# Kernel optimization log

Measured on AMD Instinct MI355X. Metric: run time of the kernel, lower is better.

## Reference

```python
import jax, jax.numpy as jnp
import numpy as np

B, T, F = 16, 2048, 512


def setup_inputs() -> dict:
    key = jax.random.key(0)
    k1, k2, k3 = jax.random.split(key, 3)
    x = jax.random.normal(k1, (B, T, F), dtype=jnp.float32)
    w_aggr = jax.random.normal(k2, (F, 1), dtype=jnp.float32) * 0.02
    b_aggr = jnp.zeros((1,), dtype=jnp.float32)
    # lengths in [T//2, T] to avoid degenerate lengths[0]==0 (torch would div by 0 too)
    seq_len = jax.random.randint(k3, (B,), T // 2, T + 1).astype(jnp.int32)
    return {"x": x, "w_aggr": w_aggr, "b_aggr": b_aggr, "seq_len": seq_len}


def reference(x, w_aggr, b_aggr, seq_len):
    """Valley-detection dynamic segment-mean pooling.

    Faithful to the torch code, but the O(T^2) triangular-mask bmm is
    expressed as the mathematically identical prefix-sum difference:
    bmm(utri[end]-utri[start], v) == cumsum(v)[end] - cumsum(v)[start].
    Output time dim is padded to T (>= dynamic max_counts); padded segment
    rows have start==end==0 -> numerator 0 / clamp -> exactly 0, matching
    the torch zero-padded `valleys` rows.
    """
    Bx, Tx, Fx = x.shape
    wt = jax.nn.sigmoid(x @ w_aggr + b_aggr)[..., 0]          # [B,T] gate weights
    before = jnp.pad(wt[:, :-1], ((0, 0), (1, 0)))            # pad 0 (sigmoid>0 => pos 0 never valley)
    after = jnp.pad(wt[:, 1:], ((0, 0), (0, 1)))              # pad 0 => pos T-1 never valley
    valley = (wt < before) & (wt < after)                     # [B,T] strict local minima
    starts_mask = valley.at[:, 0].set(True)                   # mask[:,0]=True
    ends_mask = valley.at[:, 0].set(False).at[:, -1].set(True)  # mask[:,0]=False; mask[:,-1]=True

    t = jnp.arange(Tx, dtype=jnp.int32)
    bi = jnp.arange(Bx)[:, None]

    def pack(m, vals):
        # left-pack values at True positions into fixed [B,T] (zeros beyond count)
        rank = jnp.cumsum(m, axis=1) - 1
        slot = jnp.where(m, rank, Tx)                         # dump non-selected into slot T
        out = jnp.zeros((Bx, Tx + 1), jnp.int32).at[bi, slot].set(vals)
        return out[:, :Tx], jnp.sum(m, axis=1)

    starts, counts = pack(starts_mask, jnp.broadcast_to(t, (Bx, Tx)))
    end_vals = jnp.broadcast_to(jnp.minimum(t + 2, Tx), (Bx, Tx))  # valley_index_end clipped to length
    ends, _ = pack(ends_mask, end_vals)

    alpha_h = wt[..., None] * x                               # [B,T,F]
    # exclusive->inclusive prefix sums with leading zero row
    cs_ah = jnp.concatenate([jnp.zeros((Bx, 1, Fx), x.dtype), jnp.cumsum(alpha_h, axis=1)], axis=1)
    cs_w = jnp.concatenate([jnp.zeros((Bx, 1), x.dtype), jnp.cumsum(wt, axis=1)], axis=1)

    num = cs_ah[bi, ends] - cs_ah[bi, starts]                 # [B,T,F] segment sums of w*x
    den = jnp.clip(cs_w[bi, ends] - cs_w[bi, starts], 1e-6, None)[..., None]
    pooled = num / den                                        # weighted segment mean

    max_counts = jnp.max(counts)
    lengths = jnp.minimum(seq_len, Tx)
    new_lengths = (lengths.astype(jnp.float32) / lengths[0].astype(jnp.float32)
                   * max_counts.astype(jnp.float32)).astype(jnp.int32)
    new_mask = t[None, :] < new_lengths[:, None]              # [B,T]
    return pooled, new_mask
```

## Files before the change

kernel.cpp:

```cpp
#include <hip/hip_runtime.h>
#include <math.h>

#define BB 16
#define TT 2048
#define FF 512

__global__ __launch_bounds__(256) void wt_kernel(const float* __restrict__ x,
                                                 const float* __restrict__ w,
                                                 const float* __restrict__ bias,
                                                 float* __restrict__ wt) {
    int gid  = blockIdx.x * 256 + threadIdx.x;
    int row  = gid >> 6;
    int lane = gid & 63;
    const float* xr = x + (size_t)row * FF + lane * 8;
    const float* wr = w + lane * 8;
    float4 a0 = *(const float4*)xr;
    float4 a1 = *(const float4*)(xr + 4);
    float4 w0 = *(const float4*)wr;
    float4 w1 = *(const float4*)(wr + 4);
    float s = a0.x * w0.x + a0.y * w0.y + a0.z * w0.z + a0.w * w0.w
            + a1.x * w1.x + a1.y * w1.y + a1.z * w1.z + a1.w * w1.w;
#pragma unroll
    for (int off = 32; off > 0; off >>= 1) s += __shfl_xor(s, off, 64);
    if (lane == 0) {
        float z = s + bias[0];
        wt[row] = 1.0f / (1.0f + expf(-z));
    }
}

__global__ __launch_bounds__(256) void seg_kernel(const float* __restrict__ wt,
                                                  int* __restrict__ starts,
                                                  int* __restrict__ ends,
                                                  int* __restrict__ counts) {
    int b   = blockIdx.x;
    int tid = threadIdx.x;
    __shared__ float sw[TT];
    __shared__ int   scan[256];
    const float* wrow = wt + b * TT;
    for (int i = tid; i < TT; i += 256) sw[i] = wrow[i];
    __syncthreads();

    int base = tid * 8;
    int flags = 0, cnt = 0;
#pragma unroll
    for (int k = 0; k < 8; ++k) {
        int t = base + k;
        bool v = (t > 0) && (t < TT - 1) && (sw[t] < sw[t - 1]) && (sw[t] < sw[t + 1]);
        if (v) { flags |= (1 << k); ++cnt; }
    }
    scan[tid] = cnt;
    __syncthreads();
    for (int off = 1; off < 256; off <<= 1) {
        int add = (tid >= off) ? scan[tid - off] : 0;
        __syncthreads();
        scan[tid] += add;
        __syncthreads();
    }
    int total = scan[255];
    int r = scan[tid] - cnt;
    int* sb = starts + b * TT;
    int* eb = ends + b * TT;
#pragma unroll
    for (int k = 0; k < 8; ++k) {
        if (flags & (1 << k)) {
            int t = base + k;
            sb[r + 1] = t;
            int e = t + 2; if (e > TT) e = TT;
            eb[r] = e;
            ++r;
        }
    }
    if (tid == 0) {
        sb[0] = 0;
        eb[total] = TT;
        counts[b] = total + 1;
    }
}

__global__ __launch_bounds__(256) void pool_kernel(const float* __restrict__ x,
                                                   const float* __restrict__ wt,
                                                   const int* __restrict__ starts,
                                                   const int* __restrict__ ends,
                                                   const int* __restrict__ counts,
                                                   float* __restrict__ out) {
    int gid  = blockIdx.x * 256 + threadIdx.x;
    int row  = gid >> 6;
    int lane = gid & 63;
    int b = row >> 11;
    int j = row & (TT - 1);
    float4 acc0 = make_float4(0.f, 0.f, 0.f, 0.f);
    float4 acc1 = make_float4(0.f, 0.f, 0.f, 0.f);
    if (j < counts[b]) {
        int s = starts[row], e = ends[row];
        const float* xb   = x + (size_t)b * TT * FF + lane * 8;
        const float* wrow = wt + b * TT;
        float den = 0.f;
        for (int t = s; t < e; ++t) {
            float wv = wrow[t];
            const float4* p = (const float4*)(xb + (size_t)t * FF);
            float4 v0 = p[0], v1 = p[1];
            acc0.x += wv * v0.x; acc0.y += wv * v0.y;
            acc0.z += wv * v0.z; acc0.w += wv * v0.w;
            acc1.x += wv * v1.x; acc1.y += wv * v1.y;
            acc1.z += wv * v1.z; acc1.w += wv * v1.w;
            den += wv;
        }
        float inv = 1.0f / fmaxf(den, 1e-6f);
        acc0.x *= inv; acc0.y *= inv; acc0.z *= inv; acc0.w *= inv;
        acc1.x *= inv; acc1.y *= inv; acc1.z *= inv; acc1.w *= inv;
    }
    float* orow = out + (size_t)row * FF + lane * 8;
    *(float4*)orow = acc0;
    *(float4*)(orow + 4) = acc1;
}

__global__ __launch_bounds__(256) void mask_kernel(const int* __restrict__ counts,
                                                   const int* __restrict__ seq_len,
                                                   float* __restrict__ mask_out) {
    int idx = blockIdx.x * 256 + threadIdx.x;
    int b = idx >> 11;
    int t = idx & (TT - 1);
    int maxc = 0;
#pragma unroll
    for (int i = 0; i < BB; ++i) maxc = max(maxc, counts[i]);
    int len_b = min(seq_len[b], TT);
    int len0  = min(seq_len[0], TT);
    int nl = (int)((float)len_b / (float)len0 * (float)maxc);
    mask_out[idx] = (t < nl) ? 1.0f : 0.0f;
}

extern "C" void kernel_launch(void* const* d_in, const int* in_sizes, int n_in,
                              void* d_out, int out_size, void* d_ws, size_t ws_size,
                              hipStream_t stream) {
    const float* x       = (const float*)d_in[0];
    const float* w_aggr  = (const float*)d_in[1];
    const float* b_aggr  = (const float*)d_in[2];
    const int*   seq_len = (const int*)d_in[3];

    float* pooled = (float*)d_out;
    float* mask   = (float*)d_out + (size_t)BB * TT * FF;

    float* wt    = (float*)d_ws;
    int* starts  = (int*)((char*)d_ws + (size_t)BB * TT * 4);
    int* ends    = starts + BB * TT;
    int* counts  = ends + BB * TT;

    const int rows = BB * TT;
    wt_kernel<<<rows / 4, 256, 0, stream>>>(x, w_aggr, b_aggr, wt);
    seg_kernel<<<BB, 256, 0, stream>>>(wt, starts, ends, counts);
    pool_kernel<<<rows / 4, 256, 0, stream>>>(x, wt, starts, ends, counts, pooled);
    mask_kernel<<<rows / 256, 256, 0, stream>>>(counts, seq_len, mask);
}
```

Before: 131.2 us.

## Rewrite segment scan as single-wavefront shuffle scan and fuse mask into pool kernel

The valley-detection kernel now uses one 64-lane wavefront per batch row. Each lane holds 32 gate values in registers, gets its neighbours through shuffles and runs a shuffle-based prefix scan, so the shared-memory scan and its __syncthreads barriers are gone. The mask computation is folded into the pool kernel as extra trailing blocks, which saves one kernel launch. The cost is a serial per-lane loop over the set bits and a larger per-thread register footprint in the seg kernel.

```diff
diff --git a/kernel.cpp b/kernel.cpp
--- a/kernel.cpp
+++ b/kernel.cpp
@@ -4,6 +4,8 @@
 #define BB 16
 #define TT 2048
 #define FF 512
+#define POOL_BLOCKS ((BB * TT) / 4)
+#define MASK_BLOCKS ((BB * TT) / 256)
 
 __global__ __launch_bounds__(256) void wt_kernel(const float* __restrict__ x,
                                                  const float* __restrict__ w,
@@ -28,62 +30,81 @@
     }
 }
 
-__global__ __launch_bounds__(256) void seg_kernel(const float* __restrict__ wt,
-                                                  int* __restrict__ starts,
-                                                  int* __restrict__ ends,
-                                                  int* __restrict__ counts) {
-    int b   = blockIdx.x;
-    int tid = threadIdx.x;
-    __shared__ float sw[TT];
-    __shared__ int   scan[256];
+__global__ __launch_bounds__(64) void seg_kernel(const float* __restrict__ wt,
+                                                 int* __restrict__ starts,
+                                                 int* __restrict__ ends,
+                                                 int* __restrict__ counts) {
+    int b    = blockIdx.x;
+    int lane = threadIdx.x;
     const float* wrow = wt + b * TT;
-    for (int i = tid; i < TT; i += 256) sw[i] = wrow[i];
-    __syncthreads();
-
-    int base = tid * 8;
-    int flags = 0, cnt = 0;
+    float v[32];
+    const float4* p = (const float4*)(wrow + lane * 32);
 #pragma unroll
     for (int k = 0; k < 8; ++k) {
-        int t = base + k;
-        bool v = (t > 0) && (t < TT - 1) && (sw[t] < sw[t - 1]) && (sw[t] < sw[t + 1]);
-        if (v) { flags |= (1 << k); ++cnt; }
+        float4 f = p[k];
+        v[4*k] = f.x; v[4*k+1] = f.y; v[4*k+2] = f.z; v[4*k+3] = f.w;
     }
-    scan[tid] = cnt;
-    __syncthreads();
-    for (int off = 1; off < 256; off <<= 1) {
-        int add = (tid >= off) ? scan[tid - off] : 0;
-        __syncthreads();
-        scan[tid] += add;
-        __syncthreads();
+    float left  = __shfl_up(v[31], 1, 64);
+    float right = __shfl_down(v[0], 1, 64);
+    unsigned int flags = 0;
+#pragma unroll
+    for (int k = 0; k < 32; ++k) {
+        int t = lane * 32 + k;
+        float prev = (k == 0)  ? left  : v[k - 1];
+        float next = (k == 31) ? right : v[k + 1];
+        bool val = (t > 0) && (t < TT - 1) && (v[k] < prev) && (v[k] < next);
+        if (val) flags |= (1u << k);
     }
-    int total = scan[255];
-    int r = scan[tid] - cnt;
+    int cnt = __popc(flags);
+    int inc = cnt;
+#pragma unroll
+    for (int off = 1; off < 64; off <<= 1) {
+        int y = __shfl_up(inc, off, 64);
+        if (lane >= off) inc += y;
+    }
+    int total = __shfl(inc, 63, 64);
+    int r = inc - cnt;
     int* sb = starts + b * TT;
     int* eb = ends + b * TT;
-#pragma unroll
-    for (int k = 0; k < 8; ++k) {
-        if (flags & (1 << k)) {
-            int t = base + k;
-            sb[r + 1] = t;
-            int e = t + 2; if (e > TT) e = TT;
-            eb[r] = e;
-            ++r;
-        }
+    unsigned int f = flags;
+    while (f) {
+        int k = __ffs(f) - 1;
+        f &= f - 1;
+        int t = lane * 32 + k;
+        sb[r + 1] = t;
+        eb[r] = t + 2;
+        ++r;
     }
-    if (tid == 0) {
+    if (lane == 0) {
         sb[0] = 0;
         eb[total] = TT;
         counts[b] = total + 1;
     }
 }
 
-__global__ __launch_bounds__(256) void pool_kernel(const float* __restrict__ x,
-                                                   const float* __restrict__ wt,
-                                                   const int* __restrict__ starts,
-                                                   const int* __restrict__ ends,
-                                                   const int* __restrict__ counts,
-                                                   float* __restrict__ out) {
-    int gid  = blockIdx.x * 256 + threadIdx.x;
+__global__ __launch_bounds__(256) void pool_mask_kernel(const float* __restrict__ x,
+                                                        const float* __restrict__ wt,
+                                                        const int* __restrict__ starts,
+                                                        const int* __restrict__ ends,
+                                                        const int* __restrict__ counts,
+                                                        const int* __restrict__ seq_len,
+                                                        float* __restrict__ out,
+                                                        float* __restrict__ mask_out) {
+    int blk = blockIdx.x;
+    if (blk >= POOL_BLOCKS) {
+        int idx = (blk - POOL_BLOCKS) * 256 + threadIdx.x;
+        int b = idx >> 11;
+        int t = idx & (TT - 1);
+        int maxc = 0;
+#pragma unroll
+        for (int i = 0; i < BB; ++i) maxc = max(maxc, counts[i]);
+        int len_b = min(seq_len[b], TT);
+        int len0  = min(seq_len[0], TT);
+        int nl = (int)((float)len_b / (float)len0 * (float)maxc);
+        mask_out[idx] = (t < nl) ? 1.0f : 0.0f;
+        return;
+    }
+    int gid  = blk * 256 + threadIdx.x;
     int row  = gid >> 6;
     int lane = gid & 63;
     int b = row >> 11;
@@ -114,21 +135,6 @@
     *(float4*)(orow + 4) = acc1;
 }
 
-__global__ __launch_bounds__(256) void mask_kernel(const int* __restrict__ counts,
-                                                   const int* __restrict__ seq_len,
-                                                   float* __restrict__ mask_out) {
-    int idx = blockIdx.x * 256 + threadIdx.x;
-    int b = idx >> 11;
-    int t = idx & (TT - 1);
-    int maxc = 0;
-#pragma unroll
-    for (int i = 0; i < BB; ++i) maxc = max(maxc, counts[i]);
-    int len_b = min(seq_len[b], TT);
-    int len0  = min(seq_len[0], TT);
-    int nl = (int)((float)len_b / (float)len0 * (float)maxc);
-    mask_out[idx] = (t < nl) ? 1.0f : 0.0f;
-}
-
 extern "C" void kernel_launch(void* const* d_in, const int* in_sizes, int n_in,
                               void* d_out, int out_size, void* d_ws, size_t ws_size,
                               hipStream_t stream) {
@@ -147,7 +153,7 @@
 
     const int rows = BB * TT;
     wt_kernel<<<rows / 4, 256, 0, stream>>>(x, w_aggr, b_aggr, wt);
-    seg_kernel<<<BB, 256, 0, stream>>>(wt, starts, ends, counts);
-    pool_kernel<<<rows / 4, 256, 0, stream>>>(x, wt, starts, ends, counts, pooled);
-    mask_kernel<<<rows / 256, 256, 0, stream>>>(counts, seq_len, mask);
+    seg_kernel<<<BB, 64, 0, stream>>>(wt, starts, ends, counts);
+    pool_mask_kernel<<<POOL_BLOCKS + MASK_BLOCKS, 256, 0, stream>>>(
+        x, wt, starts, ends, counts, seq_len, pooled, mask);
 }
```

Measured after the change: 128.7 us. Within noise of the previous version (-1.9%).

## Fuse segmentation, pooling and mask into one kernel with per-block valley scan

Applied to the files above, without the earlier changes.

Replaces the separate segmentation, pooling and mask kernels with one fused kernel. Each pooling block recomputes its batch row's valley flags and prefix scan in shared memory using wave shuffles, then finds its segment bounds by binary search. This removes the starts/ends workspace round trip, two launches and the serialized 16-block scan kernel. Block 0 computes the counts and writes the mask. Rows at index 1024 and above get nontemporal zero stores, because valleys cannot be adjacent and so there are at most 1024 segments. The cost is redundant scan work repeated in every block.

```diff
diff --git a/kernel.cpp b/kernel.cpp
--- a/kernel.cpp
+++ b/kernel.cpp
@@ -4,6 +4,9 @@
 #define BB 16
 #define TT 2048
 #define FF 512
+#define POOL_BLOCKS 8192
+
+typedef float v4f __attribute__((ext_vector_type(4)));
 
 __global__ __launch_bounds__(256) void wt_kernel(const float* __restrict__ x,
                                                  const float* __restrict__ w,
@@ -28,105 +31,133 @@
     }
 }
 
-__global__ __launch_bounds__(256) void seg_kernel(const float* __restrict__ wt,
-                                                  int* __restrict__ starts,
-                                                  int* __restrict__ ends,
-                                                  int* __restrict__ counts) {
-    int b   = blockIdx.x;
+__global__ __launch_bounds__(256) void pool_mask_kernel(const float* __restrict__ x,
+                                                        const float* __restrict__ wt,
+                                                        const int* __restrict__ seq_len,
+                                                        float* __restrict__ out,
+                                                        float* __restrict__ mask_out) {
+    int blk = blockIdx.x;
     int tid = threadIdx.x;
+
+    if (blk == 0) {
+        __shared__ int cnt16[BB];
+        __shared__ int nl16[BB];
+        if (tid < BB) cnt16[tid] = 0;
+        __syncthreads();
+        int br = tid >> 4;
+        int t0 = (tid & 15) * 128;
+        const float* wr = wt + br * TT;
+        int c = 0;
+        for (int k = 0; k < 128; ++k) {
+            int t = t0 + k;
+            if (t > 0 && t < TT - 1) {
+                float cv = wr[t];
+                if (cv < wr[t - 1] && cv < wr[t + 1]) ++c;
+            }
+        }
+        atomicAdd(&cnt16[br], c);
+        __syncthreads();
+        int maxc = 0;
+#pragma unroll
+        for (int i = 0; i < BB; ++i) maxc = max(maxc, cnt16[i] + 1);
+        if (tid < BB) {
+            int len_b = min(seq_len[tid], TT);
+            int len0  = min(seq_len[0], TT);
+            nl16[tid] = (int)((float)len_b / (float)len0 * (float)maxc);
+        }
+        __syncthreads();
+        for (int i = tid; i < BB * TT; i += 256) {
+            int bb = i >> 11, t = i & (TT - 1);
+            mask_out[i] = (t < nl16[bb]) ? 1.0f : 0.0f;
+        }
+        return;
+    }
+
+    int pb   = blk - 1;
+    int b    = pb >> 9;
+    int j0   = (pb & 511) * 4;
+    int lane = tid & 63;
+    int wv   = tid >> 6;
+    int row  = b * TT + j0 + wv;
+    float* orow = out + (size_t)row * FF + lane * 8;
+    v4f zero = (v4f)(0.f);
+
+    if (j0 >= 1024) {
+        __builtin_nontemporal_store(zero, (v4f*)orow);
+        __builtin_nontemporal_store(zero, (v4f*)(orow + 4));
+        return;
+    }
+
     __shared__ float sw[TT];
-    __shared__ int   scan[256];
+    __shared__ int   sflag[256];
+    __shared__ int   sexcl[256];
+    __shared__ int   swsum[4];
     const float* wrow = wt + b * TT;
-    for (int i = tid; i < TT; i += 256) sw[i] = wrow[i];
+    ((v4f*)sw)[tid]       = ((const v4f*)wrow)[tid];
+    ((v4f*)sw)[tid + 256] = ((const v4f*)wrow)[tid + 256];
     __syncthreads();
 
+    unsigned int flags = 0;
     int base = tid * 8;
-    int flags = 0, cnt = 0;
 #pragma unroll
     for (int k = 0; k < 8; ++k) {
         int t = base + k;
-        bool v = (t > 0) && (t < TT - 1) && (sw[t] < sw[t - 1]) && (sw[t] < sw[t + 1]);
-        if (v) { flags |= (1 << k); ++cnt; }
+        float c = sw[t];
+        bool v = (t > 0) && (t < TT - 1) && (c < sw[t - 1]) && (c < sw[t + 1]);
+        if (v) flags |= (1u << k);
     }
-    scan[tid] = cnt;
+    int cnt = __popc(flags);
+    sflag[tid] = (int)flags;
+    int inc = cnt;
+#pragma unroll
+    for (int off = 1; off < 64; off <<= 1) {
+        int y = __shfl_up(inc, off, 64);
+        if (lane >= off) inc += y;
+    }
+    if (lane == 63) swsum[wv] = inc;
+    sexcl[tid] = inc - cnt;
     __syncthreads();
-    for (int off = 1; off < 256; off <<= 1) {
-        int add = (tid >= off) ? scan[tid - off] : 0;
-        __syncthreads();
-        scan[tid] += add;
-        __syncthreads();
-    }
-    int total = scan[255];
-    int r = scan[tid] - cnt;
-    int* sb = starts + b * TT;
-    int* eb = ends + b * TT;
-#pragma unroll
-    for (int k = 0; k < 8; ++k) {
-        if (flags & (1 << k)) {
-            int t = base + k;
-            sb[r + 1] = t;
-            int e = t + 2; if (e > TT) e = TT;
-            eb[r] = e;
-            ++r;
-        }
-    }
-    if (tid == 0) {
-        sb[0] = 0;
-        eb[total] = TT;
-        counts[b] = total + 1;
-    }
-}
+    int woff = 0;
+    for (int i = 0; i < 4; ++i) if (i < wv) woff += swsum[i];
+    int myexcl = sexcl[tid] + woff;
+    __syncthreads();
+    sexcl[tid] = myexcl;
+    __syncthreads();
+    int Vtot = sexcl[255] + __popc((unsigned)sflag[255]);
 
-__global__ __launch_bounds__(256) void pool_kernel(const float* __restrict__ x,
-                                                   const float* __restrict__ wt,
-                                                   const int* __restrict__ starts,
-                                                   const int* __restrict__ ends,
-                                                   const int* __restrict__ counts,
-                                                   float* __restrict__ out) {
-    int gid  = blockIdx.x * 256 + threadIdx.x;
-    int row  = gid >> 6;
-    int lane = gid & 63;
-    int b = row >> 11;
-    int j = row & (TT - 1);
-    float4 acc0 = make_float4(0.f, 0.f, 0.f, 0.f);
-    float4 acc1 = make_float4(0.f, 0.f, 0.f, 0.f);
-    if (j < counts[b]) {
-        int s = starts[row], e = ends[row];
-        const float* xb   = x + (size_t)b * TT * FF + lane * 8;
-        const float* wrow = wt + b * TT;
+    int j = j0 + wv;
+    v4f acc0 = (v4f)(0.f);
+    v4f acc1 = (v4f)(0.f);
+    bool active = (j <= Vtot);
+    if (active) {
+        auto nth_valley = [&](int rho) -> int {
+            int lo = 0, hi = 255;
+            while (lo < hi) {
+                int mid = (lo + hi + 1) >> 1;
+                if (sexcl[mid] <= rho) lo = mid; else hi = mid - 1;
+            }
+            unsigned int f = (unsigned)sflag[lo];
+            int r = rho - sexcl[lo];
+            while (r--) f &= f - 1;
+            return lo * 8 + (__ffs(f) - 1);
+        };
+        int s = (j == 0) ? 0 : nth_valley(j - 1);
+        int e = (j < Vtot) ? nth_valley(j) + 2 : TT;
+        const float* xb = x + (size_t)b * TT * FF + lane * 8;
         float den = 0.f;
         for (int t = s; t < e; ++t) {
-            float wv = wrow[t];
-            const float4* p = (const float4*)(xb + (size_t)t * FF);
-            float4 v0 = p[0], v1 = p[1];
-            acc0.x += wv * v0.x; acc0.y += wv * v0.y;
-            acc0.z += wv * v0.z; acc0.w += wv * v0.w;
-            acc1.x += wv * v1.x; acc1.y += wv * v1.y;
-            acc1.z += wv * v1.z; acc1.w += wv * v1.w;
-            den += wv;
+            float wvv = sw[t];
+            const v4f* p = (const v4f*)(xb + (size_t)t * FF);
+            v4f v0 = p[0], v1 = p[1];
+            acc0 += wvv * v0;
+            acc1 += wvv * v1;
+            den += wvv;
         }
-        float inv = 1.0f / fmaxf(den, 1e-6f);
-        acc0.x *= inv; acc0.y *= inv; acc0.z *= inv; acc0.w *= inv;
-        acc1.x *= inv; acc1.y *= inv; acc1.z *= inv; acc1.w *= inv;
+        float invd = 1.0f / fmaxf(den, 1e-6f);
+        acc0 *= invd; acc1 *= invd;
     }
-    float* orow = out + (size_t)row * FF + lane * 8;
-    *(float4*)orow = acc0;
-    *(float4*)(orow + 4) = acc1;
-}
-
-__global__ __launch_bounds__(256) void mask_kernel(const int* __restrict__ counts,
-                                                   const int* __restrict__ seq_len,
-                                                   float* __restrict__ mask_out) {
-    int idx = blockIdx.x * 256 + threadIdx.x;
-    int b = idx >> 11;
-    int t = idx & (TT - 1);
-    int maxc = 0;
-#pragma unroll
-    for (int i = 0; i < BB; ++i) maxc = max(maxc, counts[i]);
-    int len_b = min(seq_len[b], TT);
-    int len0  = min(seq_len[0], TT);
-    int nl = (int)((float)len_b / (float)len0 * (float)maxc);
-    mask_out[idx] = (t < nl) ? 1.0f : 0.0f;
+    __builtin_nontemporal_store(acc0, (v4f*)orow);
+    __builtin_nontemporal_store(acc1, (v4f*)(orow + 4));
 }
 
 extern "C" void kernel_launch(void* const* d_in, const int* in_sizes, int n_in,
@@ -140,14 +171,8 @@
     float* pooled = (float*)d_out;
     float* mask   = (float*)d_out + (size_t)BB * TT * FF;
 
-    float* wt    = (float*)d_ws;
-    int* starts  = (int*)((char*)d_ws + (size_t)BB * TT * 4);
-    int* ends    = starts + BB * TT;
-    int* counts  = ends + BB * TT;
+    float* wt = (float*)d_ws;
 
-    const int rows = BB * TT;
-    wt_kernel<<<rows / 4, 256, 0, stream>>>(x, w_aggr, b_aggr, wt);
-    seg_kernel<<<BB, 256, 0, stream>>>(wt, starts, ends, counts);
-    pool_kernel<<<rows / 4, 256, 0, stream>>>(x, wt, starts, ends, counts, pooled);
-    mask_kernel<<<rows / 256, 256, 0, stream>>>(counts, seq_len, mask);
+    wt_kernel<<<(BB * TT) / 4, 256, 0, stream>>>(x, w_aggr, b_aggr, wt);
+    pool_mask_kernel<<<POOL_BLOCKS + 1, 256, 0, stream>>>(x, wt, seq_len, pooled, mask);
 }
```

Measured after the change: 151.1 us. +15.2%, slower.
